# Performance work log

Measured on AMD Instinct MI355X. Metric: run time of the kernel, lower is better.

The kernel has to match this reference:

```python
import jax, jax.numpy as jnp
import numpy as np

EMBED = 384
HEADS = 7
HEAD_SIZE = EMBED // HEADS  # 54; concat dim = 378 != 384 (faithful to source)
SEQ = 512
BATCH = 64
FFN = 6 * EMBED
EPS = 1e-5


def _layernorm(x, g, b):
    mu = jnp.mean(x, axis=-1, keepdims=True)
    var = jnp.mean((x - mu) ** 2, axis=-1, keepdims=True)
    return (x - mu) * jax.lax.rsqrt(var + EPS) * g + b


def setup_inputs() -> dict:
    key = jax.random.key(0)
    ks = jax.random.split(key, 14)
    s = 0.02
    return {
        "x": jax.random.normal(ks[0], (BATCH, SEQ, EMBED), jnp.float32),
        # per-head q/k/v projections stacked over heads: [H, EMBED, HEAD_SIZE]
        "wq": jax.random.normal(ks[1], (HEADS, EMBED, HEAD_SIZE), jnp.float32) * s,
        "bq": jnp.zeros((HEADS, HEAD_SIZE), jnp.float32),
        "wk": jax.random.normal(ks[2], (HEADS, EMBED, HEAD_SIZE), jnp.float32) * s,
        "bk": jnp.zeros((HEADS, HEAD_SIZE), jnp.float32),
        "wv": jax.random.normal(ks[3], (HEADS, EMBED, HEAD_SIZE), jnp.float32) * s,
        "bv": jnp.zeros((HEADS, HEAD_SIZE), jnp.float32),
        "wo": jax.random.normal(ks[4], (HEADS * HEAD_SIZE, EMBED), jnp.float32) * s,
        "bo": jnp.zeros((EMBED,), jnp.float32),
        "w1": jax.random.normal(ks[5], (EMBED, FFN), jnp.float32) * s,
        "b1": jnp.zeros((FFN,), jnp.float32),
        "w2": jax.random.normal(ks[6], (FFN, EMBED), jnp.float32) * s,
        "b2": jnp.zeros((EMBED,), jnp.float32),
        "ln1_g": jnp.ones((EMBED,), jnp.float32),
        "ln1_b": jnp.zeros((EMBED,), jnp.float32),
        "ln2_g": jnp.ones((EMBED,), jnp.float32),
        "ln2_b": jnp.zeros((EMBED,), jnp.float32),
    }


def reference(x, wq, bq, wk, bk, wv, bv, wo, bo, w1, b1, w2, b2, ln1_g, ln1_b, ln2_g, ln2_b):
    B, S, D = x.shape
    # --- multi-head causal self-attention (pre-LN) ---
    h = _layernorm(x, ln1_g, ln1_b)
    q = jnp.einsum("bsd,hdk->bhsk", h, wq) + bq[None, :, None, :]
    k = jnp.einsum("bsd,hdk->bhsk", h, wk) + bk[None, :, None, :]
    v = jnp.einsum("bsd,hdk->bhsk", h, wv) + bv[None, :, None, :]
    scale = HEAD_SIZE ** -0.5
    scores = jnp.einsum("bhsk,bhtk->bhst", q, k) * scale  # [B,H,S,S]
    causal = jnp.tril(jnp.ones((S, S), dtype=bool))
    scores = jnp.where(causal, scores, jnp.float32(-jnp.inf))
    attn = jax.nn.softmax(scores, axis=-1)
    o = jnp.einsum("bhst,bhtk->bhsk", attn, v)  # [B,H,S,hs]
    o = jnp.transpose(o, (0, 2, 1, 3)).reshape(B, S, HEADS * HEAD_SIZE)
    x = x + o @ wo + bo  # dropout = identity (eval)
    # --- feed-forward (pre-LN), exact GELU ---
    h2 = _layernorm(x, ln2_g, ln2_b)
    ff = jax.nn.gelu(h2 @ w1 + b1, approximate=False) @ w2 + b2
    return x + ff
```

## Files before the change

### kernel.cpp

```cpp
#include <hip/hip_runtime.h>
#include <hip/hip_bf16.h>
#include <cmath>

#define BATCH 64
#define SEQ   512
#define EMBED 384
#define HEADS 7
#define HSZ   54
#define FFND  2304
#define NTOK  (BATCH*SEQ)
#define QKVN  1152
#define EPS   1e-5f
#define SCALE 0.13608276348795434f

typedef __attribute__((ext_vector_type(8))) short s16x8;
typedef __attribute__((ext_vector_type(4))) float f32x4;

__device__ __forceinline__ ushort f2bf(float f) {
  __hip_bfloat16 h = __float2bfloat16(f);
  return *reinterpret_cast<ushort*>(&h);
}

__device__ __forceinline__ void gload16(const void* g, void* l) {
  __builtin_amdgcn_global_load_lds((const __attribute__((address_space(1))) void*)g,
                                   (__attribute__((address_space(3))) void*)l, 16, 0, 0);
}

__global__ __launch_bounds__(256) void ln_bf16_kernel(const float* __restrict__ x,
    const float* __restrict__ g, const float* __restrict__ b, ushort* __restrict__ out) {
  int wave = threadIdx.x >> 6, lane = threadIdx.x & 63;
  int row = (blockIdx.x << 2) + wave;
  const float* xr = x + (size_t)row * EMBED;
  float v[6]; float s = 0.f;
#pragma unroll
  for (int i = 0; i < 6; ++i) { v[i] = xr[lane + (i << 6)]; s += v[i]; }
#pragma unroll
  for (int off = 32; off; off >>= 1) s += __shfl_xor(s, off);
  float mu = s * (1.f / EMBED);
  float var = 0.f;
#pragma unroll
  for (int i = 0; i < 6; ++i) { float d = v[i] - mu; var += d * d; }
#pragma unroll
  for (int off = 32; off; off >>= 1) var += __shfl_xor(var, off);
  float rstd = rsqrtf(var * (1.f / EMBED) + EPS);
  ushort* orow = out + (size_t)row * EMBED;
#pragma unroll
  for (int i = 0; i < 6; ++i) {
    int c = lane + (i << 6);
    orow[c] = f2bf((v[i] - mu) * rstd * g[c] + b[c]);
  }
}

__global__ __launch_bounds__(256) void convT_tiled(const float* __restrict__ in,
    ushort* __restrict__ out, int K, int N, int srcK, int srcN) {
  __shared__ float t[32][33];
  int k0 = blockIdx.x << 5, n0 = blockIdx.y << 5;
  int tx = threadIdx.x & 31, ty = threadIdx.x >> 5;
#pragma unroll
  for (int i = 0; i < 4; ++i) {
    int r = ty + i * 8;
    int k = k0 + r, n = n0 + tx;
    t[r][tx] = (k < srcK && n < srcN) ? in[(size_t)k * srcN + n] : 0.f;
  }
  __syncthreads();
#pragma unroll
  for (int i = 0; i < 4; ++i) {
    int r = ty + i * 8;
    int n = n0 + r, k = k0 + tx;
    if (n < N && k < K) out[(size_t)n * K + k] = f2bf(t[tx][r]);
  }
}

__global__ __launch_bounds__(256) void conv_qkvw_tiled(const float* __restrict__ wq,
    const float* __restrict__ wk, const float* __restrict__ wv, ushort* __restrict__ wt) {
  __shared__ float t[32][33];
  int k0 = blockIdx.x << 5, hs0 = blockIdx.y << 5;
  int z = blockIdx.z, type = z / 7, h = z - type * 7;
  const float* W = (type == 0) ? wq : (type == 1) ? wk : wv;
  int tx = threadIdx.x & 31, ty = threadIdx.x >> 5;
#pragma unroll
  for (int i = 0; i < 4; ++i) {
    int r = ty + i * 8;
    int k = k0 + r, hs = hs0 + tx;
    t[r][tx] = (hs < HSZ) ? W[((size_t)h * EMBED + k) * HSZ + hs] : 0.f;
  }
  __syncthreads();
#pragma unroll
  for (int i = 0; i < 4; ++i) {
    int r = ty + i * 8;
    int hs = hs0 + r, k = k0 + tx;
    if (hs < HSZ) wt[(size_t)(type * 378 + h * HSZ + hs) * EMBED + k0 + tx] = f2bf(t[tx][r]);
  }
}

__global__ __launch_bounds__(256) void fill_misc(const float* __restrict__ bq,
    const float* __restrict__ bk, const float* __restrict__ bv,
    ushort* __restrict__ wt, float* __restrict__ bqkv) {
  int idx = blockIdx.x * 256 + threadIdx.x;
  if (idx < 18 * EMBED) wt[1134 * EMBED + idx] = 0;
  if (idx < QKVN) {
    float bval = 0.f;
    if (idx < 1134) {
      int type = idx / 378, rem = idx - type * 378;
      int h = rem / HSZ, hs = rem - h * HSZ;
      const float* B = (type == 0) ? bq : (type == 1) ? bk : bv;
      bval = B[h * HSZ + hs];
    }
    bqkv[idx] = bval;
  }
}

__global__ __launch_bounds__(256) void pad_aout_kernel(ushort* __restrict__ aout) {
  int idx = blockIdx.x * 256 + threadIdx.x;
  if (idx >= NTOK * 6) return;
  int row = idx / 6, c = idx - row * 6;
  aout[(size_t)row * EMBED + 378 + c] = 0;
}

__global__ __launch_bounds__(512) void attn_mfma_kernel(const ushort* __restrict__ qkv,
    ushort* __restrict__ o) {
  __shared__ ushort Qsh[8192];
  __shared__ ushort Ks[2][4096];
  __shared__ ushort Vt[2][4096];
  int tid = threadIdx.x;
  int id = blockIdx.x;
  int xcd = id & 7;
  int sseq = id >> 3;
  int bh = xcd + 8 * (sseq >> 2);
  int qb = 3 - (sseq & 3);
  int b = bh / HEADS, h = bh - b * HEADS;
  int qr0 = qb << 7;
  int ntile = 2 * qb + 2;
  int w = tid >> 6, l = tid & 63;
  int lr = l & 15, lg = l >> 4;
  const ushort* base = qkv + (size_t)b * SEQ * QKVN + h * HSZ;
  const size_t TSTR = (size_t)64 * QKVN * 2;

  int grow = w * 8 + (l >> 3);
  int gc = (l & 7) ^ (l >> 3);
  const char* kg  = (const char*)(base + 378 + (size_t)grow * QKVN + gc * 8);
  const char* qg0 = (const char*)(base + (size_t)(qr0 + grow) * QKVN + gc * 8);
  const char* qg1 = (const char*)(base + (size_t)(qr0 + 64 + grow) * QKVN + gc * 8);
  int vdst[4]; const char* vsrc[4]; bool vpar[4];
#pragma unroll
  for (int i = 0; i < 4; ++i) {
    int e = tid + i * 512;
    int ev = e >> 1, par = e & 1;
    int p = ev / 28, cv = ev - p * 28;
    if (cv < 27 && p < 32) {
      int k0 = 2 * p;
      int s0 = ((k0 >> 5) << 5) | (((k0 >> 2) & 3) << 3) | (((k0 >> 4) & 1) << 2) | (k0 & 3);
      int d = 2 * cv + par;
      vdst[i] = d * 64 + (s0 ^ ((d & 7) << 3));
      vsrc[i] = (const char*)(base + 756 + (size_t)(2 * p + par) * QKVN + 2 * cv);
      vpar[i] = (par != 0);
    } else { vdst[i] = -1; vsrc[i] = (const char*)base; vpar[i] = false; }
  }

  gload16(qg0, (char*)Qsh + w * 1024);
  gload16(qg1, (char*)Qsh + 8192 + w * 1024);
  gload16(kg, (char*)&Ks[0][0] + w * 1024);
  uint uv[4];
#pragma unroll
  for (int i = 0; i < 4; ++i)
    uv[i] = (vdst[i] >= 0) ? *reinterpret_cast<const uint*>(vsrc[i]) : 0u;
  __syncthreads();
  for (int e = tid; e < 640; e += 512) {
    int r = e / 5, which = e - r * 5;
    int idx = (which == 0) ? (r * 64 + ((6 ^ (r & 7)) << 3) + 6)
                           : (r * 64 + ((7 ^ (r & 7)) << 3) + 2 * (which - 1));
    *reinterpret_cast<uint*>(&Qsh[idx]) = 0;
  }
#pragma unroll
  for (int i = 0; i < 4; ++i) {
    uint u = uv[i]; uint uo = __shfl_xor(u, 1);
    if (vdst[i] >= 0) {
      uint wv2 = vpar[i] ? ((uo >> 16) | (u & 0xffff0000u)) : ((u & 0xffffu) | (uo << 16));
      *reinterpret_cast<uint*>(&Vt[0][vdst[i]]) = wv2;
    }
  }
  __syncthreads();
  int qrow = w * 16 + lr;
  s16x8 qf[2];
  qf[0] = *reinterpret_cast<const s16x8*>(&Qsh[qrow * 64 + ((8 * lg) ^ ((qrow & 7) << 3))]);
  qf[1] = *reinterpret_cast<const s16x8*>(&Qsh[qrow * 64 + ((32 + 8 * lg) ^ ((qrow & 7) << 3))]);

  int qglob = qr0 + qrow;
  float mrow = -1e30f, lrow = 0.f;
  f32x4 acc[4];
#pragma unroll
  for (int d = 0; d < 4; ++d) acc[d] = (f32x4){0.f, 0.f, 0.f, 0.f};

  for (int kt = 0; kt < ntile; ++kt) {
    int cur = kt & 1, nxt = cur ^ 1;
    if (kt + 1 < ntile) {
      kg += TSTR;
      gload16(kg, (char*)&Ks[nxt][0] + w * 1024);
#pragma unroll
      for (int i = 0; i < 4; ++i) {
        vsrc[i] += TSTR;
        if (vdst[i] >= 0) uv[i] = *reinterpret_cast<const uint*>(vsrc[i]);
      }
    }
    bool active = (kt * 64) <= (qr0 + w * 16 + 15);
    if (active) {
      bool diag = (kt * 64 + 63) > (qr0 + w * 16);
      f32x4 sacc[4];
      __builtin_amdgcn_s_setprio(1);
#pragma unroll
      for (int kb = 0; kb < 4; ++kb) {
        sacc[kb] = (f32x4){0.f, 0.f, 0.f, 0.f};
#pragma unroll
        for (int h2 = 0; h2 < 2; ++h2) {
          int row = kb * 16 + lr;
          s16x8 kf = *reinterpret_cast<const s16x8*>(
              &Ks[cur][row * 64 + ((32 * h2 + 8 * lg) ^ ((row & 7) << 3))]);
          sacc[kb] = __builtin_amdgcn_mfma_f32_16x16x32_bf16(kf, qf[h2], sacc[kb], 0, 0, 0);
        }
      }
      __builtin_amdgcn_s_setprio(0);
      float sv[4][4];
      float mt = -1e30f;
#pragma unroll
      for (int kb = 0; kb < 4; ++kb)
#pragma unroll
        for (int r = 0; r < 4; ++r) {
          float s = sacc[kb][r] * SCALE;
          if (diag && (kt * 64 + kb * 16 + 4 * lg + r) > qglob) s = -1e30f;
          sv[kb][r] = s;
          mt = fmaxf(mt, s);
        }
      mt = fmaxf(mt, __shfl_xor(mt, 16));
      mt = fmaxf(mt, __shfl_xor(mt, 32));
      if (!__all(mt - mrow <= 8.f)) {
        float mnew = fmaxf(mrow, mt);
        float al = __expf(mrow - mnew);
#pragma unroll
        for (int d = 0; d < 4; ++d)
#pragma unroll
          for (int r = 0; r < 4; ++r) acc[d][r] *= al;
        lrow *= al;
        mrow = mnew;
      }
      union { short s[16]; s16x8 v[2]; } pp;
      float lsum = 0.f;
#pragma unroll
      for (int kb = 0; kb < 4; ++kb)
#pragma unroll
        for (int r = 0; r < 4; ++r) {
          float p = __expf(sv[kb][r] - mrow);
          lsum += p;
          pp.s[kb * 4 + r] = (short)f2bf(p);
        }
      lrow += lsum;
      __builtin_amdgcn_s_setprio(1);
#pragma unroll
      for (int m = 0; m < 2; ++m)
#pragma unroll
        for (int d = 0; d < 4; ++d) {
          int row = d * 16 + lr;
          s16x8 vf = *reinterpret_cast<const s16x8*>(
              &Vt[cur][row * 64 + ((32 * m + 8 * lg) ^ ((row & 7) << 3))]);
          acc[d] = __builtin_amdgcn_mfma_f32_16x16x32_bf16(vf, pp.v[m], acc[d], 0, 0, 0);
        }
      __builtin_amdgcn_s_setprio(0);
    }
    if (kt + 1 < ntile) {
#pragma unroll
      for (int i = 0; i < 4; ++i) {
        uint u = uv[i]; uint uo = __shfl_xor(u, 1);
        if (vdst[i] >= 0) {
          uint wv2 = vpar[i] ? ((uo >> 16) | (u & 0xffff0000u)) : ((u & 0xffffu) | (uo << 16));
          *reinterpret_cast<uint*>(&Vt[nxt][vdst[i]]) = wv2;
        }
      }
      __syncthreads();
    }
  }

  lrow += __shfl_xor(lrow, 16);
  lrow += __shfl_xor(lrow, 32);
  float linv = 1.f / lrow;
  ushort* Olds = Qsh;
#pragma unroll
  for (int d = 0; d < 4; ++d)
#pragma unroll
    for (int r = 0; r < 4; ++r)
      Olds[(d * 16 + 4 * lg + r) * 128 + w * 16 + lr] = f2bf(acc[d][r] * linv);
  __syncthreads();
  for (int e = tid; e < 128 * 27; e += 512) {
    int q = e / 27, c = e - q * 27;
    uint lo = Olds[(2 * c) * 128 + q];
    uint hi = Olds[(2 * c + 1) * 128 + q];
    *reinterpret_cast<uint*>(&o[(size_t)(b * SEQ + qr0 + q) * EMBED + h * HSZ + 2 * c]) =
        lo | (hi << 16);
  }
}

template<int KSTEPS, int LDA, int LDB, int MODE, int NY>
__global__ __launch_bounds__(256) void mfma_gemm(
    const char* __restrict__ Ab, const char* __restrict__ Btb,
    const float* __restrict__ bias, const float* __restrict__ resid,
    char* __restrict__ Cb, int ncols) {
  __shared__ ushort sh[32768];
  int tid = threadIdx.x;
  int id = blockIdx.x;
  int xcd = id & 7, t = id >> 3;
  int group = t / (4 * NY), rres = t - group * (4 * NY);
  int ytile = rres >> 2, xi = rres & 3;
  int tok0 = (xcd * 32 + group * 4 + xi) << 7;
  int col0 = ytile << 7;
  int wv = tid >> 6, l = tid & 63;
  int wr = wv >> 1, wc = wv & 1;
  int lr = l & 15, lg = l >> 4;

  const char* aptr[4]; const char* bptr[4];
#pragma unroll
  for (int is = 0; is < 4; ++is) {
    int i = is * 256 + tid;
    int row = i >> 3;
    int boff = (i & 7) << 4;
    int sw = boff ^ ((row & 7) << 4);
    aptr[is] = Ab + (size_t)(tok0 + row) * LDA + sw;
    bptr[is] = Btb + (size_t)(col0 + row) * LDB + sw;
  }

  int offA[2][4], offB[2][4];
#pragma unroll
  for (int m = 0; m < 4; ++m) {
    int rowa = wr * 64 + m * 16 + lr;
    int rowb = wc * 64 + m * 16 + lr;
    int sa = (rowa & 7) << 4, sb = (rowb & 7) << 4;
#pragma unroll
    for (int kk = 0; kk < 2; ++kk) {
      int kb = kk * 64 + lg * 16;
      offA[kk][m] = (rowa * 128 + (kb ^ sa)) >> 1;
      offB[kk][m] = (rowb * 128 + (kb ^ sb)) >> 1;
    }
  }

  f32x4 acc[4][4];
#pragma unroll
  for (int m = 0; m < 4; ++m)
#pragma unroll
    for (int n = 0; n < 4; ++n) acc[m][n] = (f32x4){0.f, 0.f, 0.f, 0.f};

#pragma unroll
  for (int is = 0; is < 4; ++is) {
    gload16(aptr[is], (char*)sh + is * 4096 + wv * 1024);
    gload16(bptr[is], (char*)sh + 32768 + is * 4096 + wv * 1024);
  }
  __syncthreads();

  for (int ks = 0; ks < KSTEPS; ++ks) {
    int buf = ks & 1;
    if (ks + 1 < KSTEPS) {
      int nb = buf ^ 1;
#pragma unroll
      for (int is = 0; is < 4; ++is) {
        gload16(aptr[is] + (size_t)(ks + 1) * 128, (char*)sh + nb * 16384 + is * 4096 + wv * 1024);
        gload16(bptr[is] + (size_t)(ks + 1) * 128, (char*)sh + 32768 + nb * 16384 + is * 4096 + wv * 1024);
      }
    }
    int ao = buf * 8192, bo = 16384 + buf * 8192;
    __builtin_amdgcn_s_setprio(1);
#pragma unroll
    for (int kk = 0; kk < 2; ++kk) {
      s16x8 af[4], bfr[4];
#pragma unroll
      for (int m = 0; m < 4; ++m) af[m] = *reinterpret_cast<const s16x8*>(&sh[ao + offA[kk][m]]);
#pragma unroll
      for (int n = 0; n < 4; ++n) bfr[n] = *reinterpret_cast<const s16x8*>(&sh[bo + offB[kk][n]]);
#pragma unroll
      for (int m = 0; m < 4; ++m)
#pragma unroll
        for (int n = 0; n < 4; ++n)
          acc[m][n] = __builtin_amdgcn_mfma_f32_16x16x32_bf16(af[m], bfr[n], acc[m][n], 0, 0, 0);
    }
    __builtin_amdgcn_s_setprio(0);
    if (ks + 1 < KSTEPS) __syncthreads();
  }

  float bn[4];
  int colr = col0 + wc * 64 + lr;
#pragma unroll
  for (int n = 0; n < 4; ++n) bn[n] = bias[colr + n * 16];

  if constexpr (MODE == 2) {
    int tokr = tok0 + wr * 64 + lg * 4;
    float* C = (float*)Cb;
#pragma unroll
    for (int m = 0; m < 4; ++m)
#pragma unroll
      for (int r = 0; r < 4; ++r) {
        size_t rowbase = (size_t)(tokr + m * 16 + r) * ncols;
#pragma unroll
        for (int n = 0; n < 4; ++n) {
          size_t idx = rowbase + colr + n * 16;
          C[idx] = acc[m][n][r] + bn[n] + resid[idx];
        }
      }
  } else {
    __syncthreads();
#pragma unroll
    for (int m = 0; m < 4; ++m)
#pragma unroll
      for (int r = 0; r < 4; ++r) {
        int row = wr * 64 + m * 16 + lg * 4 + r;
        int rmask = ((row >> 2) & 3) << 4;
#pragma unroll
        for (int n = 0; n < 4; ++n) {
          float xg = acc[m][n][r] + bn[n];
          if constexpr (MODE == 1) {
            float u2 = xg * (1.5957691216f + 0.0713548162f * xg * xg);
            xg = xg * __builtin_amdgcn_rcpf(1.f + __expf(-u2));
          }
          int col = wc * 64 + n * 16 + lr;
          sh[row * 128 + (col ^ rmask)] = f2bf(xg);
        }
      }
    __syncthreads();
    ushort* C = (ushort*)Cb;
    int blk = (l & 7) + 8 * (wv & 1);
    int rbase = (l >> 3) + 64 * (wv >> 1);
#pragma unroll
    for (int it = 0; it < 8; ++it) {
      int row = rbase + 8 * it;
      int pblk = blk ^ (((row >> 2) & 3) << 1);
      uint4 vvv = *reinterpret_cast<const uint4*>(&sh[row * 128 + pblk * 8]);
      *reinterpret_cast<uint4*>(&C[(size_t)(tok0 + row) * ncols + col0 + blk * 8]) = vvv;
    }
  }
}

extern "C" void kernel_launch(void* const* d_in, const int* in_sizes, int n_in,
                              void* d_out, int out_size, void* d_ws, size_t ws_size,
                              hipStream_t stream) {
  const float* x    = (const float*)d_in[0];
  const float* wq   = (const float*)d_in[1];
  const float* bq   = (const float*)d_in[2];
  const float* wk   = (const float*)d_in[3];
  const float* bk   = (const float*)d_in[4];
  const float* wv   = (const float*)d_in[5];
  const float* bv   = (const float*)d_in[6];
  const float* wo   = (const float*)d_in[7];
  const float* bo   = (const float*)d_in[8];
  const float* w1   = (const float*)d_in[9];
  const float* b1   = (const float*)d_in[10];
  const float* w2   = (const float*)d_in[11];
  const float* b2   = (const float*)d_in[12];
  const float* ln1g = (const float*)d_in[13];
  const float* ln1b = (const float*)d_in[14];
  const float* ln2g = (const float*)d_in[15];
  const float* ln2b = (const float*)d_in[16];
  float* out = (float*)d_out;

  char* wsb = (char*)d_ws;
  float*  x1    = (float*)wsb;
  ushort* ffnb  = (ushort*)(wsb + 50331648);
  ushort* hb    = (ushort*)(wsb + 50331648);
  ushort* qkvb  = (ushort*)(wsb + 75497472);
  ushort* aout  = (ushort*)(wsb + 150994944);
  ushort* h2b   = (ushort*)(wsb + 201326592);
  ushort* w1t   = (ushort*)(wsb + 226492416);
  ushort* w2t   = (ushort*)(wsb + 228261888);
  ushort* wqkvt = (ushort*)(wsb + 230031360);
  ushort* wot   = (ushort*)(wsb + 230916096);
  float*  bqkv  = (float*)(wsb + 231211008);

  conv_qkvw_tiled<<<dim3(12, 2, 21), 256, 0, stream>>>(wq, wk, wv, wqkvt);
  fill_misc      <<<27, 256, 0, stream>>>(bq, bk, bv, wqkvt, bqkv);
  convT_tiled    <<<dim3(12, 12), 256, 0, stream>>>(wo, wot, EMBED, EMBED, 378, EMBED);
  convT_tiled    <<<dim3(12, 72), 256, 0, stream>>>(w1, w1t, EMBED, FFND, EMBED, FFND);
  convT_tiled    <<<dim3(72, 12), 256, 0, stream>>>(w2, w2t, FFND, EMBED, FFND, EMBED);
  pad_aout_kernel<<<(NTOK * 6 + 255) / 256, 256, 0, stream>>>(aout);

  ln_bf16_kernel<<<NTOK / 4, 256, 0, stream>>>(x, ln1g, ln1b, hb);
  mfma_gemm<EMBED / 64, EMBED * 2, EMBED * 2, 0, QKVN / 128>
      <<<256 * (QKVN / 128), 256, 0, stream>>>(
      (const char*)hb, (const char*)wqkvt, bqkv, nullptr, (char*)qkvb, QKVN);
  attn_mfma_kernel<<<BATCH * HEADS * 4, 512, 0, stream>>>(qkvb, aout);
  mfma_gemm<EMBED / 64, EMBED * 2, EMBED * 2, 2, EMBED / 128>
      <<<256 * (EMBED / 128), 256, 0, stream>>>(
      (const char*)aout, (const char*)wot, bo, x, (char*)x1, EMBED);
  ln_bf16_kernel<<<NTOK / 4, 256, 0, stream>>>(x1, ln2g, ln2b, h2b);
  mfma_gemm<EMBED / 64, EMBED * 2, EMBED * 2, 1, FFND / 128>
      <<<256 * (FFND / 128), 256, 0, stream>>>(
      (const char*)h2b, (const char*)w1t, b1, nullptr, (char*)ffnb, FFND);
  mfma_gemm<FFND / 64, FFND * 2, FFND * 2, 2, EMBED / 128>
      <<<256 * (EMBED / 128), 256, 0, stream>>>(
      (const char*)ffnb, (const char*)w2t, b2, x1, (char*)out, EMBED);
}
```

Measured before the change: 383.0 us.

## Fuse LayerNorm into GEMM A-load, merge prep kernels, fold softmax scale into Wq

Removes the standalone LayerNorm kernels. The QKV and FFN1 GEMMs now read fp32 activations, compute per-row mean/rstd in-block, and normalize and convert to bf16 while staging the A tile into LDS. All weight-conversion and padding kernels are merged into one launch. The softmax scale and log2(e) are folded into the Q weights and bias so attention can use a raw exp2 and skip a multiply. This trades the LN write/read round-trips for redundant per-block statistic recomputation, doubled fp32 A traffic, and register-path loads instead of direct-to-LDS loads.

```diff
diff --git a/kernel.cpp b/kernel.cpp
--- a/kernel.cpp
+++ b/kernel.cpp
@@ -11,7 +11,8 @@
 #define NTOK  (BATCH*SEQ)
 #define QKVN  1152
 #define EPS   1e-5f
-#define SCALE 0.13608276348795434f
+#define LAM   0.19632593f
+#define THR2  11.5415603f
 
 typedef __attribute__((ext_vector_type(8))) short s16x8;
 typedef __attribute__((ext_vector_type(4))) float f32x4;
@@ -21,41 +22,19 @@
   return *reinterpret_cast<ushort*>(&h);
 }
 
+__device__ __forceinline__ float exp2fast(float f) {
+  return __builtin_amdgcn_exp2f(f);
+}
+
 __device__ __forceinline__ void gload16(const void* g, void* l) {
   __builtin_amdgcn_global_load_lds((const __attribute__((address_space(1))) void*)g,
                                    (__attribute__((address_space(3))) void*)l, 16, 0, 0);
 }
 
-__global__ __launch_bounds__(256) void ln_bf16_kernel(const float* __restrict__ x,
-    const float* __restrict__ g, const float* __restrict__ b, ushort* __restrict__ out) {
-  int wave = threadIdx.x >> 6, lane = threadIdx.x & 63;
-  int row = (blockIdx.x << 2) + wave;
-  const float* xr = x + (size_t)row * EMBED;
-  float v[6]; float s = 0.f;
-#pragma unroll
-  for (int i = 0; i < 6; ++i) { v[i] = xr[lane + (i << 6)]; s += v[i]; }
-#pragma unroll
-  for (int off = 32; off; off >>= 1) s += __shfl_xor(s, off);
-  float mu = s * (1.f / EMBED);
-  float var = 0.f;
-#pragma unroll
-  for (int i = 0; i < 6; ++i) { float d = v[i] - mu; var += d * d; }
-#pragma unroll
-  for (int off = 32; off; off >>= 1) var += __shfl_xor(var, off);
-  float rstd = rsqrtf(var * (1.f / EMBED) + EPS);
-  ushort* orow = out + (size_t)row * EMBED;
-#pragma unroll
-  for (int i = 0; i < 6; ++i) {
-    int c = lane + (i << 6);
-    orow[c] = f2bf((v[i] - mu) * rstd * g[c] + b[c]);
-  }
-}
-
-__global__ __launch_bounds__(256) void convT_tiled(const float* __restrict__ in,
-    ushort* __restrict__ out, int K, int N, int srcK, int srcN) {
-  __shared__ float t[32][33];
-  int k0 = blockIdx.x << 5, n0 = blockIdx.y << 5;
-  int tx = threadIdx.x & 31, ty = threadIdx.x >> 5;
+__device__ __forceinline__ void convT_body(const float* __restrict__ in,
+    ushort* __restrict__ out, int K, int N, int srcK, int srcN,
+    int k0, int n0, int tid, float (*t)[33]) {
+  int tx = tid & 31, ty = tid >> 5;
 #pragma unroll
   for (int i = 0; i < 4; ++i) {
     int r = ty + i * 8;
@@ -71,50 +50,66 @@
   }
 }
 
-__global__ __launch_bounds__(256) void conv_qkvw_tiled(const float* __restrict__ wq,
-    const float* __restrict__ wk, const float* __restrict__ wv, ushort* __restrict__ wt) {
+__global__ __launch_bounds__(256) void prep_all(
+    const float* __restrict__ wq, const float* __restrict__ wk, const float* __restrict__ wv,
+    const float* __restrict__ bq, const float* __restrict__ bk, const float* __restrict__ bv,
+    const float* __restrict__ wo, const float* __restrict__ w1, const float* __restrict__ w2,
+    ushort* __restrict__ wqkvt, ushort* __restrict__ wot,
+    ushort* __restrict__ w1t, ushort* __restrict__ w2t,
+    float* __restrict__ bqkv, ushort* __restrict__ aout) {
   __shared__ float t[32][33];
-  int k0 = blockIdx.x << 5, hs0 = blockIdx.y << 5;
-  int z = blockIdx.z, type = z / 7, h = z - type * 7;
-  const float* W = (type == 0) ? wq : (type == 1) ? wk : wv;
-  int tx = threadIdx.x & 31, ty = threadIdx.x >> 5;
-#pragma unroll
-  for (int i = 0; i < 4; ++i) {
-    int r = ty + i * 8;
-    int k = k0 + r, hs = hs0 + tx;
-    t[r][tx] = (hs < HSZ) ? W[((size_t)h * EMBED + k) * HSZ + hs] : 0.f;
-  }
-  __syncthreads();
-#pragma unroll
-  for (int i = 0; i < 4; ++i) {
-    int r = ty + i * 8;
-    int hs = hs0 + r, k = k0 + tx;
-    if (hs < HSZ) wt[(size_t)(type * 378 + h * HSZ + hs) * EMBED + k0 + tx] = f2bf(t[tx][r]);
-  }
-}
-
-__global__ __launch_bounds__(256) void fill_misc(const float* __restrict__ bq,
-    const float* __restrict__ bk, const float* __restrict__ bv,
-    ushort* __restrict__ wt, float* __restrict__ bqkv) {
-  int idx = blockIdx.x * 256 + threadIdx.x;
-  if (idx < 18 * EMBED) wt[1134 * EMBED + idx] = 0;
-  if (idx < QKVN) {
-    float bval = 0.f;
-    if (idx < 1134) {
-      int type = idx / 378, rem = idx - type * 378;
-      int h = rem / HSZ, hs = rem - h * HSZ;
-      const float* B = (type == 0) ? bq : (type == 1) ? bk : bv;
-      bval = B[h * HSZ + hs];
-    }
-    bqkv[idx] = bval;
-  }
-}
-
-__global__ __launch_bounds__(256) void pad_aout_kernel(ushort* __restrict__ aout) {
-  int idx = blockIdx.x * 256 + threadIdx.x;
-  if (idx >= NTOK * 6) return;
-  int row = idx / 6, c = idx - row * 6;
-  aout[(size_t)row * EMBED + 378 + c] = 0;
+  int bid = blockIdx.x, tid = threadIdx.x;
+  if (bid < 504) {
+    int z = bid / 24, rem = bid - z * 24;
+    int k0 = (rem >> 1) << 5, hs0 = (rem & 1) << 5;
+    int type = z / 7, h = z - type * 7;
+    const float* W = (type == 0) ? wq : (type == 1) ? wk : wv;
+    float lam = (type == 0) ? LAM : 1.f;
+    int tx = tid & 31, ty = tid >> 5;
+#pragma unroll
+    for (int i = 0; i < 4; ++i) {
+      int r = ty + i * 8;
+      int k = k0 + r, hs = hs0 + tx;
+      t[r][tx] = (hs < HSZ) ? W[((size_t)h * EMBED + k) * HSZ + hs] : 0.f;
+    }
+    __syncthreads();
+#pragma unroll
+    for (int i = 0; i < 4; ++i) {
+      int r = ty + i * 8;
+      int hs = hs0 + r;
+      if (hs < HSZ)
+        wqkvt[(size_t)(type * 378 + h * HSZ + hs) * EMBED + k0 + tx] = f2bf(t[tx][r] * lam);
+    }
+  } else if (bid < 531) {
+    int idx = (bid - 504) * 256 + tid;
+    if (idx < 18 * EMBED) wqkvt[1134 * EMBED + idx] = 0;
+    if (idx < QKVN) {
+      float bval = 0.f;
+      if (idx < 1134) {
+        int type = idx / 378, rem = idx - type * 378;
+        int h = rem / HSZ, hs = rem - h * HSZ;
+        const float* B = (type == 0) ? bq : (type == 1) ? bk : bv;
+        bval = B[h * HSZ + hs];
+        if (type == 0) bval *= LAM;
+      }
+      bqkv[idx] = bval;
+    }
+  } else if (bid < 675) {
+    int r = bid - 531;
+    convT_body(wo, wot, EMBED, EMBED, 378, EMBED, (r / 12) << 5, (r % 12) << 5, tid, t);
+  } else if (bid < 1539) {
+    int r = bid - 675;
+    convT_body(w1, w1t, EMBED, FFND, EMBED, FFND, (r % 12) << 5, (r / 12) << 5, tid, t);
+  } else if (bid < 2403) {
+    int r = bid - 1539;
+    convT_body(w2, w2t, FFND, EMBED, FFND, EMBED, (r % 72) << 5, (r / 72) << 5, tid, t);
+  } else {
+    int idx = (bid - 2403) * 256 + tid;
+    if (idx < NTOK * 6) {
+      int row = idx / 6, c = idx - row * 6;
+      aout[(size_t)row * EMBED + 378 + c] = 0;
+    }
+  }
 }
 
 __global__ __launch_bounds__(512) void attn_mfma_kernel(const ushort* __restrict__ qkv,
@@ -225,16 +220,16 @@
       for (int kb = 0; kb < 4; ++kb)
 #pragma unroll
         for (int r = 0; r < 4; ++r) {
-          float s = sacc[kb][r] * SCALE;
+          float s = sacc[kb][r];
           if (diag && (kt * 64 + kb * 16 + 4 * lg + r) > qglob) s = -1e30f;
           sv[kb][r] = s;
           mt = fmaxf(mt, s);
         }
       mt = fmaxf(mt, __shfl_xor(mt, 16));
       mt = fmaxf(mt, __shfl_xor(mt, 32));
-      if (!__all(mt - mrow <= 8.f)) {
+      if (!__all(mt - mrow <= THR2)) {
         float mnew = fmaxf(mrow, mt);
-        float al = __expf(mrow - mnew);
+        float al = exp2fast(mrow - mnew);
 #pragma unroll
         for (int d = 0; d < 4; ++d)
 #pragma unroll
@@ -248,7 +243,7 @@
       for (int kb = 0; kb < 4; ++kb)
 #pragma unroll
         for (int r = 0; r < 4; ++r) {
-          float p = __expf(sv[kb][r] - mrow);
+          float p = exp2fast(sv[kb][r] - mrow);
           lsum += p;
           pp.s[kb * 4 + r] = (short)f2bf(p);
         }
@@ -297,12 +292,16 @@
   }
 }
 
-template<int KSTEPS, int LDA, int LDB, int MODE, int NY>
+template<int KSTEPS, int LDA, int LDB, int MODE, int NY, bool LNA>
 __global__ __launch_bounds__(256) void mfma_gemm(
     const char* __restrict__ Ab, const char* __restrict__ Btb,
     const float* __restrict__ bias, const float* __restrict__ resid,
-    char* __restrict__ Cb, int ncols) {
+    char* __restrict__ Cb, int ncols,
+    const float* __restrict__ lng, const float* __restrict__ lnb) {
   __shared__ ushort sh[32768];
+  __shared__ float mu_s[128], rs_s[128];
+  __shared__ __align__(16) float gbg[384];
+  __shared__ __align__(16) float gbb[384];
   int tid = threadIdx.x;
   int id = blockIdx.x;
   int xcd = id & 7, t = id >> 3;
@@ -315,6 +314,7 @@
   int lr = l & 15, lg = l >> 4;
 
   const char* aptr[4]; const char* bptr[4];
+  int arow[4], asc[4];
 #pragma unroll
   for (int is = 0; is < 4; ++is) {
     int i = is * 256 + tid;
@@ -323,6 +323,8 @@
     int sw = boff ^ ((row & 7) << 4);
     aptr[is] = Ab + (size_t)(tok0 + row) * LDA + sw;
     bptr[is] = Btb + (size_t)(col0 + row) * LDB + sw;
+    arow[is] = row;
+    asc[is] = (i & 7) ^ (row & 7);
   }
 
   int offA[2][4], offB[2][4];
@@ -345,21 +347,85 @@
 #pragma unroll
     for (int n = 0; n < 4; ++n) acc[m][n] = (f32x4){0.f, 0.f, 0.f, 0.f};
 
-#pragma unroll
-  for (int is = 0; is < 4; ++is) {
-    gload16(aptr[is], (char*)sh + is * 4096 + wv * 1024);
+  const float* Xf = (const float*)Ab;
+  float amu[4], ars[4];
+  float4 preA[4][2];
+
+#pragma unroll
+  for (int is = 0; is < 4; ++is)
     gload16(bptr[is], (char*)sh + 32768 + is * 4096 + wv * 1024);
+
+  if constexpr (LNA) {
+    for (int rr = 0; rr < 32; ++rr) {
+      int row = wv * 32 + rr;
+      const float* xr = Xf + (size_t)(tok0 + row) * (LDA / 4);
+      float v[6]; float s = 0.f;
+#pragma unroll
+      for (int i = 0; i < 6; ++i) { v[i] = xr[l + (i << 6)]; s += v[i]; }
+#pragma unroll
+      for (int off = 32; off; off >>= 1) s += __shfl_xor(s, off);
+      float mu = s * (1.f / EMBED);
+      float var = 0.f;
+#pragma unroll
+      for (int i = 0; i < 6; ++i) { float d = v[i] - mu; var += d * d; }
+#pragma unroll
+      for (int off = 32; off; off >>= 1) var += __shfl_xor(var, off);
+      if (l == 0) { mu_s[row] = mu; rs_s[row] = rsqrtf(var * (1.f / EMBED) + EPS); }
+    }
+    for (int c = tid; c < 384; c += 256) { gbg[c] = lng[c]; gbb[c] = lnb[c]; }
+    __syncthreads();
+#pragma unroll
+    for (int is = 0; is < 4; ++is) { amu[is] = mu_s[arow[is]]; ars[is] = rs_s[arow[is]]; }
+#pragma unroll
+    for (int is = 0; is < 4; ++is) {
+      const float* src = Xf + (size_t)(tok0 + arow[is]) * (LDA / 4) + asc[is] * 8;
+      preA[is][0] = *reinterpret_cast<const float4*>(src);
+      preA[is][1] = *reinterpret_cast<const float4*>(src + 4);
+    }
+#pragma unroll
+    for (int is = 0; is < 4; ++is) {
+      int c0 = asc[is] * 8;
+      float4 gA = *reinterpret_cast<const float4*>(&gbg[c0]);
+      float4 gB = *reinterpret_cast<const float4*>(&gbg[c0 + 4]);
+      float4 bA = *reinterpret_cast<const float4*>(&gbb[c0]);
+      float4 bB = *reinterpret_cast<const float4*>(&gbb[c0 + 4]);
+      float mu = amu[is], rs = ars[is];
+      uint4 pk;
+      pk.x = (uint)f2bf((preA[is][0].x - mu) * rs * gA.x + bA.x) |
+             ((uint)f2bf((preA[is][0].y - mu) * rs * gA.y + bA.y) << 16);
+      pk.y = (uint)f2bf((preA[is][0].z - mu) * rs * gA.z + bA.z) |
+             ((uint)f2bf((preA[is][0].w - mu) * rs * gA.w + bA.w) << 16);
+      pk.z = (uint)f2bf((preA[is][1].x - mu) * rs * gB.x + bB.x) |
+             ((uint)f2bf((preA[is][1].y - mu) * rs * gB.y + bB.y) << 16);
+      pk.w = (uint)f2bf((preA[is][1].z - mu) * rs * gB.z + bB.z) |
+             ((uint)f2bf((preA[is][1].w - mu) * rs * gB.w + bB.w) << 16);
+      *reinterpret_cast<uint4*>((char*)sh + is * 4096 + wv * 1024 + l * 16) = pk;
+    }
+  } else {
+#pragma unroll
+    for (int is = 0; is < 4; ++is)
+      gload16(aptr[is], (char*)sh + is * 4096 + wv * 1024);
   }
   __syncthreads();
 
   for (int ks = 0; ks < KSTEPS; ++ks) {
     int buf = ks & 1;
+    int nb = buf ^ 1;
     if (ks + 1 < KSTEPS) {
-      int nb = buf ^ 1;
-#pragma unroll
-      for (int is = 0; is < 4; ++is) {
-        gload16(aptr[is] + (size_t)(ks + 1) * 128, (char*)sh + nb * 16384 + is * 4096 + wv * 1024);
+#pragma unroll
+      for (int is = 0; is < 4; ++is)
         gload16(bptr[is] + (size_t)(ks + 1) * 128, (char*)sh + 32768 + nb * 16384 + is * 4096 + wv * 1024);
+      if constexpr (LNA) {
+#pragma unroll
+        for (int is = 0; is < 4; ++is) {
+          const float* src = Xf + (size_t)(tok0 + arow[is]) * (LDA / 4) + (ks + 1) * 64 + asc[is] * 8;
+          preA[is][0] = *reinterpret_cast<const float4*>(src);
+          preA[is][1] = *reinterpret_cast<const float4*>(src + 4);
+        }
+      } else {
+#pragma unroll
+        for (int is = 0; is < 4; ++is)
+          gload16(aptr[is] + (size_t)(ks + 1) * 128, (char*)sh + nb * 16384 + is * 4096 + wv * 1024);
       }
     }
     int ao = buf * 8192, bo = 16384 + buf * 8192;
@@ -378,7 +444,30 @@
           acc[m][n] = __builtin_amdgcn_mfma_f32_16x16x32_bf16(af[m], bfr[n], acc[m][n], 0, 0, 0);
     }
     __builtin_amdgcn_s_setprio(0);
-    if (ks + 1 < KSTEPS) __syncthreads();
+    if (ks + 1 < KSTEPS) {
+      if constexpr (LNA) {
+#pragma unroll
+        for (int is = 0; is < 4; ++is) {
+          int c0 = (ks + 1) * 64 + asc[is] * 8;
+          float4 gA = *reinterpret_cast<const float4*>(&gbg[c0]);
+          float4 gB = *reinterpret_cast<const float4*>(&gbg[c0 + 4]);
+          float4 bA = *reinterpret_cast<const float4*>(&gbb[c0]);
+          float4 bB = *reinterpret_cast<const float4*>(&gbb[c0 + 4]);
+          float mu = amu[is], rs = ars[is];
+          uint4 pk;
+          pk.x = (uint)f2bf((preA[is][0].x - mu) * rs * gA.x + bA.x) |
+                 ((uint)f2bf((preA[is][0].y - mu) * rs * gA.y + bA.y) << 16);
+          pk.y = (uint)f2bf((preA[is][0].z - mu) * rs * gA.z + bA.z) |
+                 ((uint)f2bf((preA[is][0].w - mu) * rs * gA.w + bA.w) << 16);
+          pk.z = (uint)f2bf((preA[is][1].x - mu) * rs * gB.x + bB.x) |
+                 ((uint)f2bf((preA[is][1].y - mu) * rs * gB.y + bB.y) << 16);
+          pk.w = (uint)f2bf((preA[is][1].z - mu) * rs * gB.z + bB.z) |
+                 ((uint)f2bf((preA[is][1].w - mu) * rs * gB.w + bB.w) << 16);
+          *reinterpret_cast<uint4*>((char*)sh + nb * 16384 + is * 4096 + wv * 1024 + l * 16) = pk;
+        }
+      }
+      __syncthreads();
+    }
   }
 
   float bn[4];
@@ -458,36 +547,27 @@
   char* wsb = (char*)d_ws;
   float*  x1    = (float*)wsb;
   ushort* ffnb  = (ushort*)(wsb + 50331648);
-  ushort* hb    = (ushort*)(wsb + 50331648);
   ushort* qkvb  = (ushort*)(wsb + 75497472);
   ushort* aout  = (ushort*)(wsb + 150994944);
-  ushort* h2b   = (ushort*)(wsb + 201326592);
   ushort* w1t   = (ushort*)(wsb + 226492416);
   ushort* w2t   = (ushort*)(wsb + 228261888);
   ushort* wqkvt = (ushort*)(wsb + 230031360);
   ushort* wot   = (ushort*)(wsb + 230916096);
   float*  bqkv  = (float*)(wsb + 231211008);
 
-  conv_qkvw_tiled<<<dim3(12, 2, 21), 256, 0, stream>>>(wq, wk, wv, wqkvt);
-  fill_misc      <<<27, 256, 0, stream>>>(bq, bk, bv, wqkvt, bqkv);
-  convT_tiled    <<<dim3(12, 12), 256, 0, stream>>>(wo, wot, EMBED, EMBED, 378, EMBED);
-  convT_tiled    <<<dim3(12, 72), 256, 0, stream>>>(w1, w1t, EMBED, FFND, EMBED, FFND);
-  convT_tiled    <<<dim3(72, 12), 256, 0, stream>>>(w2, w2t, FFND, EMBED, FFND, EMBED);
-  pad_aout_kernel<<<(NTOK * 6 + 255) / 256, 256, 0, stream>>>(aout);
-
-  ln_bf16_kernel<<<NTOK / 4, 256, 0, stream>>>(x, ln1g, ln1b, hb);
-  mfma_gemm<EMBED / 64, EMBED * 2, EMBED * 2, 0, QKVN / 128>
+  prep_all<<<3171, 256, 0, stream>>>(wq, wk, wv, bq, bk, bv, wo, w1, w2,
+                                     wqkvt, wot, w1t, w2t, bqkv, aout);
+  mfma_gemm<EMBED / 64, EMBED * 4, EMBED * 2, 0, QKVN / 128, true>
       <<<256 * (QKVN / 128), 256, 0, stream>>>(
-      (const char*)hb, (const char*)wqkvt, bqkv, nullptr, (char*)qkvb, QKVN);
+      (const char*)x, (const char*)wqkvt, bqkv, nullptr, (char*)qkvb, QKVN, ln1g, ln1b);
   attn_mfma_kernel<<<BATCH * HEADS * 4, 512, 0, stream>>>(qkvb, aout);
-  mfma_gemm<EMBED / 64, EMBED * 2, EMBED * 2, 2, EMBED / 128>
+  mfma_gemm<EMBED / 64, EMBED * 2, EMBED * 2, 2, EMBED / 128, false>
       <<<256 * (EMBED / 128), 256, 0, stream>>>(
-      (const char*)aout, (const char*)wot, bo, x, (char*)x1, EMBED);
-  ln_bf16_kernel<<<NTOK / 4, 256, 0, stream>>>(x1, ln2g, ln2b, h2b);
-  mfma_gemm<EMBED / 64, EMBED * 2, EMBED * 2, 1, FFND / 128>
+      (const char*)aout, (const char*)wot, bo, x, (char*)x1, EMBED, nullptr, nullptr);
+  mfma_gemm<EMBED / 64, EMBED * 4, EMBED * 2, 1, FFND / 128, true>
       <<<256 * (FFND / 128), 256, 0, stream>>>(
-      (const char*)h2b, (const char*)w1t, b1, nullptr, (char*)ffnb, FFND);
-  mfma_gemm<FFND / 64, FFND * 2, FFND * 2, 2, EMBED / 128>
+      (const char*)x1, (const char*)w1t, b1, nullptr, (char*)ffnb, FFND, ln2g, ln2b);
+  mfma_gemm<FFND / 64, FFND * 2, FFND * 2, 2, EMBED / 128, false>
       <<<256 * (EMBED / 128), 256, 0, stream>>>(
-      (const char*)ffnb, (const char*)w2t, b2, x1, (char*)out, EMBED);
-}
+      (const char*)ffnb, (const char*)w2t, b2, x1, (char*)out, EMBED, nullptr, nullptr);
+}
```

New measurement: 1.118 ms. 2.92x slower.

## Merge weight-prep kernels into one launch and fold softmax scale into Wq

Applied to the files above, without the earlier changes.

Six small setup kernels (QKV weight transpose, bias fill, three weight transposes, aout padding) become a single prep_all kernel that dispatches on block index, removing five launches. The query weights and bias are pre-multiplied by scale*log2(e), so attention drops the per-score multiply and uses the hardware exp2 instead of __expf; the rescale threshold is adjusted to match. This slightly changes bf16 rounding of the scaled Q weights.

```diff
diff --git a/kernel.cpp b/kernel.cpp
--- a/kernel.cpp
+++ b/kernel.cpp
@@ -11,7 +11,8 @@
 #define NTOK  (BATCH*SEQ)
 #define QKVN  1152
 #define EPS   1e-5f
-#define SCALE 0.13608276348795434f
+#define LAM   0.19632593f
+#define THR2  11.5415603f
 
 typedef __attribute__((ext_vector_type(8))) short s16x8;
 typedef __attribute__((ext_vector_type(4))) float f32x4;
@@ -19,6 +20,10 @@
 __device__ __forceinline__ ushort f2bf(float f) {
   __hip_bfloat16 h = __float2bfloat16(f);
   return *reinterpret_cast<ushort*>(&h);
+}
+
+__device__ __forceinline__ float exp2fast(float f) {
+  return __builtin_amdgcn_exp2f(f);
 }
 
 __device__ __forceinline__ void gload16(const void* g, void* l) {
@@ -51,11 +56,10 @@
   }
 }
 
-__global__ __launch_bounds__(256) void convT_tiled(const float* __restrict__ in,
-    ushort* __restrict__ out, int K, int N, int srcK, int srcN) {
-  __shared__ float t[32][33];
-  int k0 = blockIdx.x << 5, n0 = blockIdx.y << 5;
-  int tx = threadIdx.x & 31, ty = threadIdx.x >> 5;
+__device__ __forceinline__ void convT_body(const float* __restrict__ in,
+    ushort* __restrict__ out, int K, int N, int srcK, int srcN,
+    int k0, int n0, int tid, float (*t)[33]) {
+  int tx = tid & 31, ty = tid >> 5;
 #pragma unroll
   for (int i = 0; i < 4; ++i) {
     int r = ty + i * 8;
@@ -71,50 +75,66 @@
   }
 }
 
-__global__ __launch_bounds__(256) void conv_qkvw_tiled(const float* __restrict__ wq,
-    const float* __restrict__ wk, const float* __restrict__ wv, ushort* __restrict__ wt) {
+__global__ __launch_bounds__(256) void prep_all(
+    const float* __restrict__ wq, const float* __restrict__ wk, const float* __restrict__ wv,
+    const float* __restrict__ bq, const float* __restrict__ bk, const float* __restrict__ bv,
+    const float* __restrict__ wo, const float* __restrict__ w1, const float* __restrict__ w2,
+    ushort* __restrict__ wqkvt, ushort* __restrict__ wot,
+    ushort* __restrict__ w1t, ushort* __restrict__ w2t,
+    float* __restrict__ bqkv, ushort* __restrict__ aout) {
   __shared__ float t[32][33];
-  int k0 = blockIdx.x << 5, hs0 = blockIdx.y << 5;
-  int z = blockIdx.z, type = z / 7, h = z - type * 7;
-  const float* W = (type == 0) ? wq : (type == 1) ? wk : wv;
-  int tx = threadIdx.x & 31, ty = threadIdx.x >> 5;
-#pragma unroll
-  for (int i = 0; i < 4; ++i) {
-    int r = ty + i * 8;
-    int k = k0 + r, hs = hs0 + tx;
-    t[r][tx] = (hs < HSZ) ? W[((size_t)h * EMBED + k) * HSZ + hs] : 0.f;
-  }
-  __syncthreads();
-#pragma unroll
-  for (int i = 0; i < 4; ++i) {
-    int r = ty + i * 8;
-    int hs = hs0 + r, k = k0 + tx;
-    if (hs < HSZ) wt[(size_t)(type * 378 + h * HSZ + hs) * EMBED + k0 + tx] = f2bf(t[tx][r]);
-  }
-}
-
-__global__ __launch_bounds__(256) void fill_misc(const float* __restrict__ bq,
-    const float* __restrict__ bk, const float* __restrict__ bv,
-    ushort* __restrict__ wt, float* __restrict__ bqkv) {
-  int idx = blockIdx.x * 256 + threadIdx.x;
-  if (idx < 18 * EMBED) wt[1134 * EMBED + idx] = 0;
-  if (idx < QKVN) {
-    float bval = 0.f;
-    if (idx < 1134) {
-      int type = idx / 378, rem = idx - type * 378;
-      int h = rem / HSZ, hs = rem - h * HSZ;
-      const float* B = (type == 0) ? bq : (type == 1) ? bk : bv;
-      bval = B[h * HSZ + hs];
-    }
-    bqkv[idx] = bval;
-  }
-}
-
-__global__ __launch_bounds__(256) void pad_aout_kernel(ushort* __restrict__ aout) {
-  int idx = blockIdx.x * 256 + threadIdx.x;
-  if (idx >= NTOK * 6) return;
-  int row = idx / 6, c = idx - row * 6;
-  aout[(size_t)row * EMBED + 378 + c] = 0;
+  int bid = blockIdx.x, tid = threadIdx.x;
+  if (bid < 504) {
+    int z = bid / 24, rem = bid - z * 24;
+    int k0 = (rem >> 1) << 5, hs0 = (rem & 1) << 5;
+    int type = z / 7, h = z - type * 7;
+    const float* W = (type == 0) ? wq : (type == 1) ? wk : wv;
+    float lam = (type == 0) ? LAM : 1.f;
+    int tx = tid & 31, ty = tid >> 5;
+#pragma unroll
+    for (int i = 0; i < 4; ++i) {
+      int r = ty + i * 8;
+      int k = k0 + r, hs = hs0 + tx;
+      t[r][tx] = (hs < HSZ) ? W[((size_t)h * EMBED + k) * HSZ + hs] : 0.f;
+    }
+    __syncthreads();
+#pragma unroll
+    for (int i = 0; i < 4; ++i) {
+      int r = ty + i * 8;
+      int hs = hs0 + r;
+      if (hs < HSZ)
+        wqkvt[(size_t)(type * 378 + h * HSZ + hs) * EMBED + k0 + tx] = f2bf(t[tx][r] * lam);
+    }
+  } else if (bid < 531) {
+    int idx = (bid - 504) * 256 + tid;
+    if (idx < 18 * EMBED) wqkvt[1134 * EMBED + idx] = 0;
+    if (idx < QKVN) {
+      float bval = 0.f;
+      if (idx < 1134) {
+        int type = idx / 378, rem = idx - type * 378;
+        int h = rem / HSZ, hs = rem - h * HSZ;
+        const float* B = (type == 0) ? bq : (type == 1) ? bk : bv;
+        bval = B[h * HSZ + hs];
+        if (type == 0) bval *= LAM;
+      }
+      bqkv[idx] = bval;
+    }
+  } else if (bid < 675) {
+    int r = bid - 531;
+    convT_body(wo, wot, EMBED, EMBED, 378, EMBED, (r / 12) << 5, (r % 12) << 5, tid, t);
+  } else if (bid < 1539) {
+    int r = bid - 675;
+    convT_body(w1, w1t, EMBED, FFND, EMBED, FFND, (r % 12) << 5, (r / 12) << 5, tid, t);
+  } else if (bid < 2403) {
+    int r = bid - 1539;
+    convT_body(w2, w2t, FFND, EMBED, FFND, EMBED, (r % 72) << 5, (r / 72) << 5, tid, t);
+  } else {
+    int idx = (bid - 2403) * 256 + tid;
+    if (idx < NTOK * 6) {
+      int row = idx / 6, c = idx - row * 6;
+      aout[(size_t)row * EMBED + 378 + c] = 0;
+    }
+  }
 }
 
 __global__ __launch_bounds__(512) void attn_mfma_kernel(const ushort* __restrict__ qkv,
@@ -225,16 +245,16 @@
       for (int kb = 0; kb < 4; ++kb)
 #pragma unroll
         for (int r = 0; r < 4; ++r) {
-          float s = sacc[kb][r] * SCALE;
+          float s = sacc[kb][r];
           if (diag && (kt * 64 + kb * 16 + 4 * lg + r) > qglob) s = -1e30f;
           sv[kb][r] = s;
           mt = fmaxf(mt, s);
         }
       mt = fmaxf(mt, __shfl_xor(mt, 16));
       mt = fmaxf(mt, __shfl_xor(mt, 32));
-      if (!__all(mt - mrow <= 8.f)) {
+      if (!__all(mt - mrow <= THR2)) {
         float mnew = fmaxf(mrow, mt);
-        float al = __expf(mrow - mnew);
+        float al = exp2fast(mrow - mnew);
 #pragma unroll
         for (int d = 0; d < 4; ++d)
 #pragma unroll
@@ -248,7 +268,7 @@
       for (int kb = 0; kb < 4; ++kb)
 #pragma unroll
         for (int r = 0; r < 4; ++r) {
-          float p = __expf(sv[kb][r] - mrow);
+          float p = exp2fast(sv[kb][r] - mrow);
           lsum += p;
           pp.s[kb * 4 + r] = (short)f2bf(p);
         }
@@ -468,13 +488,8 @@
   ushort* wot   = (ushort*)(wsb + 230916096);
   float*  bqkv  = (float*)(wsb + 231211008);
 
-  conv_qkvw_tiled<<<dim3(12, 2, 21), 256, 0, stream>>>(wq, wk, wv, wqkvt);
-  fill_misc      <<<27, 256, 0, stream>>>(bq, bk, bv, wqkvt, bqkv);
-  convT_tiled    <<<dim3(12, 12), 256, 0, stream>>>(wo, wot, EMBED, EMBED, 378, EMBED);
-  convT_tiled    <<<dim3(12, 72), 256, 0, stream>>>(w1, w1t, EMBED, FFND, EMBED, FFND);
-  convT_tiled    <<<dim3(72, 12), 256, 0, stream>>>(w2, w2t, FFND, EMBED, FFND, EMBED);
-  pad_aout_kernel<<<(NTOK * 6 + 255) / 256, 256, 0, stream>>>(aout);
-
+  prep_all<<<3171, 256, 0, stream>>>(wq, wk, wv, bq, bk, bv, wo, w1, w2,
+                                     wqkvt, wot, w1t, w2t, bqkv, aout);
   ln_bf16_kernel<<<NTOK / 4, 256, 0, stream>>>(x, ln1g, ln1b, hb);
   mfma_gemm<EMBED / 64, EMBED * 2, EMBED * 2, 0, QKVN / 128>
       <<<256 * (QKVN / 128), 256, 0, stream>>>(
```

After: 365.5 us. 4.5% less time.
